# Performance work log

Measured on AMD Instinct MI355X. Metric: run time of the kernel, lower is better.

The kernel has to match this reference:

```python
import jax, jax.numpy as jnp
import numpy as np

TAU = 0.5

def setup_inputs() -> dict:
    key = jax.random.key(0)
    ks = jax.random.split(key, 6)
    B, L, D, P = 4, 4096, 256, 256
    return {
        "X1": jax.random.normal(ks[0], (B, L, D), dtype=jnp.float32),
        "X2": jax.random.normal(ks[1], (B, L, D), dtype=jnp.float32),
        "W1": jax.random.normal(ks[2], (P, D), dtype=jnp.float32) * (1.0 / np.sqrt(D)),
        "b1": jax.random.normal(ks[3], (P,), dtype=jnp.float32) * 0.01,
        "W2": jax.random.normal(ks[4], (D, P), dtype=jnp.float32) * (1.0 / np.sqrt(P)),
        "b2": jax.random.normal(ks[5], (D,), dtype=jnp.float32) * 0.01,
    }

def _projection(z, W1, b1, W2, b2):
    h = jax.nn.elu(z @ W1.T + b1)
    return h @ W2.T + b2

def _normalize(z, eps=1e-12):
    n = jnp.linalg.norm(z, axis=-1, keepdims=True)
    return z / jnp.maximum(n, eps)

def _semi_loss(z1, z2, tau):
    # z1, z2: [B, L, D]
    z1n = _normalize(z1)
    z2n = _normalize(z2)
    refl = jnp.exp(jnp.einsum('bld,bmd->blm', z1n, z1n) / tau)   # [B, L, L]
    between = jnp.exp(jnp.einsum('bld,bmd->blm', z1n, z2n) / tau)
    refl_diag = jnp.diagonal(refl, axis1=-2, axis2=-1)           # [B, L]
    between_diag = jnp.diagonal(between, axis1=-2, axis2=-1)
    denom = refl.sum(axis=-1) + between.sum(axis=-1) - refl_diag
    return -jnp.log(between_diag / denom).sum(axis=-1)           # [B]

def reference(X1, X2, W1, b1, W2, b2):
    h1 = _projection(X1, W1, b1, W2, b2)
    h2 = _projection(X2, W1, b1, W2, b2)
    l1 = _semi_loss(h1, h2, TAU)
    l2 = _semi_loss(h2, h1, TAU)
    return ((l1 + l2) * 0.5).mean()
```

## Files before the change

kernel.cpp:

```cpp
#include <hip/hip_runtime.h>
#include <math.h>


typedef __attribute__((ext_vector_type(8))) short short8;
typedef __attribute__((ext_vector_type(4))) short short4v;
typedef __attribute__((ext_vector_type(4))) float float4v;
typedef __attribute__((ext_vector_type(8))) int int8v;
typedef __attribute__((ext_vector_type(4))) int int4v;

__device__ __forceinline__ short f2bf(float f) {
    unsigned u = __builtin_bit_cast(unsigned, f);
    u += 0x7fffu + ((u >> 16) & 1u);
    return (short)(u >> 16);
}

__device__ __forceinline__ unsigned char f2fp8(float f) {
    float af = fabsf(f);
    unsigned s = (__builtin_bit_cast(unsigned, f) >> 31) << 7;
    if (af < 0.015625f) {
        int q = (int)rintf(af * 512.0f);
        return (unsigned char)(s | (unsigned)q);
    }
    unsigned au = __builtin_bit_cast(unsigned, af);
    au += 0x7FFFFu + ((au >> 20) & 1u);
    int e = (int)(au >> 23) - 127;
    unsigned m = (au >> 20) & 7u;
    return (unsigned char)(s | (unsigned)((e + 7) << 3) | m);
}

__device__ __forceinline__ void gl_lds16(const void* g, void* l) {
    __builtin_amdgcn_global_load_lds(
        (const __attribute__((address_space(1))) void*)g,
        (__attribute__((address_space(3))) void*)l, 16, 0, 0);
}

__device__ __forceinline__ void gemm256_core(
    const short* __restrict__ A, const short* __restrict__ B,
    int arow0, short* lsA, short* lsB, float4v acc[4][4])
{
    const int tid  = threadIdx.x;
    const int w    = tid >> 6;
    const int lane = tid & 63;
    const int l15  = lane & 15;

    for (int kt = 0; kt < 4; ++kt) {
        const int kbase = kt * 64;
#pragma unroll
        for (int r = 0; r < 10; ++r) {
            const int c = w * 10 + r;
            if (c < 8) {
                const int s   = c * 64 + lane;
                const int kc  = s >> 6;
                const int row = s & 63;
                gl_lds16(A + (size_t)(arow0 + row) * 256 + kbase + kc * 8,
                         lsA + (size_t)c * 512);
            } else {
                const int s   = (c - 8) * 64 + lane;
                const int kc  = s >> 8;
                const int row = s & 255;
                gl_lds16(B + (size_t)row * 256 + kbase + kc * 8,
                         lsB + (size_t)(c - 8) * 512);
            }
        }
        __syncthreads();
#pragma unroll
        for (int ks = 0; ks < 2; ++ks) {
            const int kc = ks * 4 + (lane >> 4);
            short8 af[4], bfv[4];
#pragma unroll
            for (int mi = 0; mi < 4; ++mi)
                af[mi] = *(const short8*)(lsA + ((size_t)kc * 64 + mi * 16 + l15) * 8);
#pragma unroll
            for (int ni = 0; ni < 4; ++ni)
                bfv[ni] = *(const short8*)(lsB + ((size_t)kc * 256 + w * 64 + ni * 16 + l15) * 8);
#pragma unroll
            for (int mi = 0; mi < 4; ++mi)
#pragma unroll
                for (int ni = 0; ni < 4; ++ni)
                    acc[mi][ni] = __builtin_amdgcn_mfma_f32_16x16x32_bf16(
                        af[mi], bfv[ni], acc[mi][ni], 0, 0, 0);
        }
        __syncthreads();
    }
}

__global__ __launch_bounds__(256) void convX_kernel(
    const float* __restrict__ X1, const float* __restrict__ X2,
    short* __restrict__ dst)
{
    int i = blockIdx.x * 256 + threadIdx.x;
    const float* src = (i < 1048576) ? X1 : X2;
    int j = i & 1048575;
    float4v v = ((const float4v*)src)[j];
    short4v o;
    o.x = f2bf(v.x); o.y = f2bf(v.y); o.z = f2bf(v.z); o.w = f2bf(v.w);
    ((short4v*)dst)[i] = o;
}

__global__ __launch_bounds__(256) void convW_kernel(
    const float* __restrict__ W1, const float* __restrict__ W2,
    short* __restrict__ d1, short* __restrict__ d2)
{
    int i = blockIdx.x * 256 + threadIdx.x;
    const float* src = (i < 16384) ? W1 : W2;
    short* dst = (i < 16384) ? d1 : d2;
    int j = i & 16383;
    float4v v = ((const float4v*)src)[j];
    short4v o;
    o.x = f2bf(v.x); o.y = f2bf(v.y); o.z = f2bf(v.z); o.w = f2bf(v.w);
    ((short4v*)dst)[j] = o;
}

__global__ __launch_bounds__(256, 4) void proj1_kernel(
    const short* __restrict__ Xbf, const short* __restrict__ W1bf,
    const float* __restrict__ b1, short* __restrict__ Hbf)
{
    __shared__ short lsA[4096];
    __shared__ short lsB[16384];
    const int arow0 = blockIdx.x * 64;
    float4v acc[4][4];
#pragma unroll
    for (int mi = 0; mi < 4; ++mi)
#pragma unroll
        for (int ni = 0; ni < 4; ++ni)
            acc[mi][ni] = (float4v){0.f, 0.f, 0.f, 0.f};

    gemm256_core(Xbf, W1bf, arow0, lsA, lsB, acc);

    const int tid  = threadIdx.x;
    const int w    = tid >> 6;
    const int lane = tid & 63;
    const int rowbase = arow0 + (lane >> 4) * 4;
    const int colbase = w * 64 + (lane & 15);
#pragma unroll
    for (int ni = 0; ni < 4; ++ni) {
        const int col = colbase + ni * 16;
        const float bv = b1[col];
#pragma unroll
        for (int mi = 0; mi < 4; ++mi)
#pragma unroll
            for (int reg = 0; reg < 4; ++reg) {
                const int row = rowbase + mi * 16 + reg;
                float v = acc[mi][ni][reg] + bv;
                v = (v > 0.f) ? v : expm1f(v);
                Hbf[(size_t)row * 256 + col] = f2bf(v);
            }
    }
}

__global__ __launch_bounds__(256, 4) void proj2norm_kernel(
    const short* __restrict__ Hbf, const short* __restrict__ W2bf,
    const float* __restrict__ b2, unsigned char* __restrict__ zn8)
{
    __shared__ short lsA[4096];
    __shared__ short lsB[16384];
    __shared__ float rssq[4][64];
    __shared__ float rinv[64];
    const int arow0 = blockIdx.x * 64;
    float4v acc[4][4];
#pragma unroll
    for (int mi = 0; mi < 4; ++mi)
#pragma unroll
        for (int ni = 0; ni < 4; ++ni)
            acc[mi][ni] = (float4v){0.f, 0.f, 0.f, 0.f};

    gemm256_core(Hbf, W2bf, arow0, lsA, lsB, acc);

    const int tid  = threadIdx.x;
    const int w    = tid >> 6;
    const int lane = tid & 63;
    const int quad = lane >> 4;
    const int l15  = lane & 15;

#pragma unroll
    for (int ni = 0; ni < 4; ++ni) {
        const float bv = b2[w * 64 + ni * 16 + l15];
#pragma unroll
        for (int mi = 0; mi < 4; ++mi)
#pragma unroll
            for (int reg = 0; reg < 4; ++reg)
                acc[mi][ni][reg] += bv;
    }
    float ps[4][4];
#pragma unroll
    for (int mi = 0; mi < 4; ++mi)
#pragma unroll
        for (int reg = 0; reg < 4; ++reg) {
            float s = 0.f;
#pragma unroll
            for (int ni = 0; ni < 4; ++ni) {
                float v = acc[mi][ni][reg];
                s += v * v;
            }
            s += __shfl_xor(s, 1); s += __shfl_xor(s, 2);
            s += __shfl_xor(s, 4); s += __shfl_xor(s, 8);
            ps[mi][reg] = s;
        }
    if (l15 == 0) {
#pragma unroll
        for (int mi = 0; mi < 4; ++mi)
#pragma unroll
            for (int reg = 0; reg < 4; ++reg)
                rssq[w][mi * 16 + quad * 4 + reg] = ps[mi][reg];
    }
    __syncthreads();
    if (tid < 64) {
        float ssq = rssq[0][tid] + rssq[1][tid] + rssq[2][tid] + rssq[3][tid];
        rinv[tid] = 1.41421356237f / fmaxf(sqrtf(ssq), 1e-12f);
    }
    __syncthreads();

    const int r0  = arow0;
    const int set = r0 >> 14;
    const int bb  = (r0 >> 12) & 3;
    const int l0  = r0 & 4095;
    unsigned char* dst = zn8 + ((size_t)(bb * 2 + set) * 4096 + l0) * 256;
    const int colbase = w * 64 + l15;
#pragma unroll
    for (int mi = 0; mi < 4; ++mi)
#pragma unroll
        for (int reg = 0; reg < 4; ++reg) {
            const int rl = mi * 16 + quad * 4 + reg;
            const float inv = rinv[rl];
#pragma unroll
            for (int ni = 0; ni < 4; ++ni)
                dst[(size_t)rl * 256 + colbase + ni * 16] =
                    f2fp8(acc[mi][ni][reg] * inv);
        }
}

#if defined(__has_builtin)
#if __has_builtin(__builtin_amdgcn_mfma_scale_f32_16x16x128_f8f6f4)
#define HAVE_MX 1
#endif
#endif

__global__ __launch_bounds__(256, 2) void gram_fp8_kernel(
    const unsigned char* __restrict__ zn8, float* __restrict__ S,
    float* __restrict__ out)
{
    __shared__ unsigned char lsB[2][32768];

    const int bx    = blockIdx.x;
    const int xcd   = bx & 7;
    const int batch = xcd >> 1;
    const int sub   = (bx >> 3) * 2 + (xcd & 1);
    const int stripe = sub >> 1;
    const int half   = sub & 1;
    const unsigned char* Z = zn8 + (size_t)batch * 2097152;
    const int q0 = stripe * 128;
    const int t0 = half * 32;
    const int djt = (q0 ^ 4096) >> 7;

    const int tid  = threadIdx.x;
    const int w    = tid >> 6;
    const int lane = tid & 63;
    const int wm   = w & 1;
    const int wn   = w >> 1;
    const int quad = lane >> 4;
    const int l15  = lane & 15;

#define STAGE_B(t, buf)                                                       \
    {                                                                         \
        const unsigned char* Bb = Z + (size_t)(t) * 128 * 256;                \
        _Pragma("unroll")                                                     \
        for (int r = 0; r < 8; ++r) {                                         \
            const int c   = w * 8 + r;                                        \
            const int u   = c * 64 + lane;                                    \
            const int kp  = u >> 7;                                           \
            const int col = u & 127;                                          \
            gl_lds16(Bb + (size_t)col * 256 + kp * 16,                        \
                     &lsB[buf][(size_t)c * 1024]);                            \
        }                                                                     \
    }

    float rs[4][4];
#pragma unroll
    for (int mi = 0; mi < 4; ++mi)
#pragma unroll
        for (int reg = 0; reg < 4; ++reg)
            rs[mi][reg] = 0.f;
    float dsum = 0.f;

#ifdef HAVE_MX
    int8v afr[4][2];
    {
        const unsigned char* Ab = Z + (size_t)(q0 + wm * 64) * 256;
#pragma unroll
        for (int mi = 0; mi < 4; ++mi)
#pragma unroll
            for (int ks = 0; ks < 2; ++ks) {
                const unsigned char* p = Ab + (size_t)(mi * 16 + l15) * 256
                                         + ks * 128 + quad * 32;
                int4v lo = *(const int4v*)p;
                int4v hi = *(const int4v*)(p + 16);
                afr[mi][ks] = __builtin_shufflevector(lo, hi, 0,1,2,3,4,5,6,7);
            }
    }

    STAGE_B(t0, 0);
    __syncthreads();

    for (int jt = 0; jt < 32; ++jt) {
        const int buf = jt & 1;
        if (jt < 31) STAGE_B(t0 + jt + 1, buf ^ 1);

        float4v acc[4][4];
#pragma unroll
        for (int mi = 0; mi < 4; ++mi)
#pragma unroll
            for (int ni = 0; ni < 4; ++ni)
                acc[mi][ni] = (float4v){0.f, 0.f, 0.f, 0.f};

        const unsigned char* lb = &lsB[buf][0];
#pragma unroll
        for (int ks = 0; ks < 2; ++ks) {
            const int kp0 = ks * 8 + quad * 2;
            int8v bfv[4];
#pragma unroll
            for (int ni = 0; ni < 4; ++ni) {
                const unsigned char* p = lb +
                    ((size_t)kp0 * 128 + wn * 64 + ni * 16 + l15) * 16;
                int4v lo = *(const int4v*)p;
                int4v hi = *(const int4v*)(p + 2048);
                bfv[ni] = __builtin_shufflevector(lo, hi, 0,1,2,3,4,5,6,7);
            }
#pragma unroll
            for (int mi = 0; mi < 4; ++mi)
#pragma unroll
                for (int ni = 0; ni < 4; ++ni)
                    acc[mi][ni] = __builtin_amdgcn_mfma_scale_f32_16x16x128_f8f6f4(
                        afr[mi][ks], bfv[ni], acc[mi][ni],
                        0, 0,
                        0, 0x7F7F7F7F,
                        0, 0x7F7F7F7F);
        }

        if (t0 + jt == djt) {
#pragma unroll
            for (int mi = 0; mi < 4; ++mi)
#pragma unroll
                for (int ni = 0; ni < 4; ++ni)
#pragma unroll
                    for (int reg = 0; reg < 4; ++reg) {
                        const int rg = q0 + wm * 64 + mi * 16 + quad * 4 + reg;
                        const int cg = djt * 128 + wn * 64 + ni * 16 + l15;
                        if ((rg ^ 4096) == cg) dsum += acc[mi][ni][reg];
                    }
        }

#pragma unroll
        for (int mi = 0; mi < 4; ++mi)
#pragma unroll
            for (int reg = 0; reg < 4; ++reg) {
                float s = 0.f;
#pragma unroll
                for (int ni = 0; ni < 4; ++ni)
                    s += __expf(acc[mi][ni][reg]);
                rs[mi][reg] += s;
            }

        __syncthreads();
    }
#else
    long afr[4][8];
    {
        const unsigned char* Ab = Z + (size_t)(q0 + wm * 64) * 256;
#pragma unroll
        for (int mi = 0; mi < 4; ++mi)
#pragma unroll
            for (int kc = 0; kc < 8; ++kc)
                afr[mi][kc] = *(const long*)(Ab + (size_t)(mi * 16 + l15) * 256
                                             + kc * 32 + quad * 8);
    }
    STAGE_B(t0, 0);
    __syncthreads();
    for (int jt = 0; jt < 32; ++jt) {
        const int buf = jt & 1;
        if (jt < 31) STAGE_B(t0 + jt + 1, buf ^ 1);
        float4v acc[4][4];
#pragma unroll
        for (int mi = 0; mi < 4; ++mi)
#pragma unroll
            for (int ni = 0; ni < 4; ++ni)
                acc[mi][ni] = (float4v){0.f, 0.f, 0.f, 0.f};
        const unsigned char* lb = &lsB[buf][0];
#pragma unroll
        for (int kc = 0; kc < 8; ++kc) {
            const int kseg = kc * 4 + quad;
            const int kp   = kseg >> 1;
            const int hf   = kseg & 1;
            long bfv[4];
#pragma unroll
            for (int ni = 0; ni < 4; ++ni)
                bfv[ni] = *(const long*)(lb +
                    ((size_t)kp * 128 + wn * 64 + ni * 16 + l15) * 16 + hf * 8);
#pragma unroll
            for (int mi = 0; mi < 4; ++mi)
#pragma unroll
                for (int ni = 0; ni < 4; ++ni)
                    acc[mi][ni] = __builtin_amdgcn_mfma_f32_16x16x32_fp8_fp8(
                        afr[mi][kc], bfv[ni], acc[mi][ni], 0, 0, 0);
        }
        if (t0 + jt == djt) {
#pragma unroll
            for (int mi = 0; mi < 4; ++mi)
#pragma unroll
                for (int ni = 0; ni < 4; ++ni)
#pragma unroll
                    for (int reg = 0; reg < 4; ++reg) {
                        const int rg = q0 + wm * 64 + mi * 16 + quad * 4 + reg;
                        const int cg = djt * 128 + wn * 64 + ni * 16 + l15;
                        if ((rg ^ 4096) == cg) dsum += acc[mi][ni][reg];
                    }
        }
#pragma unroll
        for (int mi = 0; mi < 4; ++mi)
#pragma unroll
            for (int reg = 0; reg < 4; ++reg) {
                float s = 0.f;
#pragma unroll
                for (int ni = 0; ni < 4; ++ni)
                    s += __expf(acc[mi][ni][reg]);
                rs[mi][reg] += s;
            }
        __syncthreads();
    }
#endif

#pragma unroll
    for (int mi = 0; mi < 4; ++mi)
#pragma unroll
        for (int reg = 0; reg < 4; ++reg) {
            float v = rs[mi][reg];
            v += __shfl_xor(v, 1); v += __shfl_xor(v, 2);
            v += __shfl_xor(v, 4); v += __shfl_xor(v, 8);
            rs[mi][reg] = v;
        }
    if (l15 == 0) {
        float* Sq = S + (size_t)batch * 8192 + q0 + wm * 64;
#pragma unroll
        for (int mi = 0; mi < 4; ++mi)
#pragma unroll
            for (int reg = 0; reg < 4; ++reg)
                atomicAdd(&Sq[mi * 16 + quad * 4 + reg], rs[mi][reg]);
    }
    {
        float dv = dsum;
        dv += __shfl_xor(dv, 1);  dv += __shfl_xor(dv, 2);
        dv += __shfl_xor(dv, 4);  dv += __shfl_xor(dv, 8);
        dv += __shfl_xor(dv, 16); dv += __shfl_xor(dv, 32);
        if (lane == 0 && dv != 0.f)
            atomicAdd(out, -0.125f * dv);
    }
#undef STAGE_B
}

__global__ __launch_bounds__(256) void final_log_kernel(
    const float* __restrict__ S, float* __restrict__ out)
{
    __shared__ float red[4];
    const int tid  = threadIdx.x;
    const int w    = tid >> 6;
    const int lane = tid & 63;
    const float E2 = 7.3890560989306495f;
    float acc = 0.f;
    for (int i = blockIdx.x * 256 + tid; i < 32768; i += gridDim.x * 256)
        acc += logf(S[i] - E2);
    acc += __shfl_xor(acc, 1);  acc += __shfl_xor(acc, 2);
    acc += __shfl_xor(acc, 4);  acc += __shfl_xor(acc, 8);
    acc += __shfl_xor(acc, 16); acc += __shfl_xor(acc, 32);
    if (lane == 0) red[w] = acc;
    __syncthreads();
    if (tid == 0)
        atomicAdd(out, 0.125f * (red[0] + red[1] + red[2] + red[3]));
}

extern "C" void kernel_launch(void* const* d_in, const int* in_sizes, int n_in,
                              void* d_out, int out_size, void* d_ws, size_t ws_size,
                              hipStream_t stream)
{
    const float* X1 = (const float*)d_in[0];
    const float* X2 = (const float*)d_in[1];
    const float* W1 = (const float*)d_in[2];
    const float* b1 = (const float*)d_in[3];
    const float* W2 = (const float*)d_in[4];
    const float* b2 = (const float*)d_in[5];

    char* ws = (char*)d_ws;
    float* S    = (float*)(ws + 0);
    short* W1bf = (short*)(ws + 131072);
    short* W2bf = (short*)(ws + 262144);
    short* Xbf  = (short*)(ws + 393216);
    unsigned char* zn8 = (unsigned char*)(ws + 393216);
    short* Hbf  = (short*)(ws + 17170432);

    hipMemsetAsync(S, 0, 131072, stream);
    hipMemsetAsync(d_out, 0, sizeof(float), stream);

    convW_kernel<<<128, 256, 0, stream>>>(W1, W2, W1bf, W2bf);
    convX_kernel<<<8192, 256, 0, stream>>>(X1, X2, Xbf);
    proj1_kernel<<<512, 256, 0, stream>>>(Xbf, W1bf, b1, Hbf);
    proj2norm_kernel<<<512, 256, 0, stream>>>(Hbf, W2bf, b2, zn8);
    gram_fp8_kernel<<<512, 256, 0, stream>>>(zn8, S, (float*)d_out);
    final_log_kernel<<<64, 256, 0, stream>>>(S, (float*)d_out);
}
```

Measured before the change: 217.3 us.

## Exploit Gram matrix symmetry with upper-triangular tiles and exp2 scaling

Replaces the row-stripe Gram kernel with one block per upper-triangular 128x128 tile of the combined 8192x8192 similarity matrix, so each off-diagonal tile's exponentials feed both its row sums and its column sums. This halves the MFMA and exp work. It also folds log2(e) into the normalisation scale so exp2 can be used directly, and rescales the diagonal term to match. The cost is many more small blocks (8320), no double-buffered staging, and roughly twice as many atomics per element. The triangular index is recovered with a sqrt plus correction loops.

New measurement: 676.2 us. +211.1%, slower.

```diff
diff --git a/kernel.cpp b/kernel.cpp
--- a/kernel.cpp
+++ b/kernel.cpp
@@ -7,6 +7,15 @@
 typedef __attribute__((ext_vector_type(4))) float float4v;
 typedef __attribute__((ext_vector_type(8))) int int8v;
 typedef __attribute__((ext_vector_type(4))) int int4v;
+
+#if defined(__has_builtin)
+#if __has_builtin(__builtin_amdgcn_exp2f)
+#define EXP2F(x) __builtin_amdgcn_exp2f(x)
+#endif
+#endif
+#ifndef EXP2F
+#define EXP2F(x) __expf(0.69314718056f * (x))
+#endif
 
 __device__ __forceinline__ short f2bf(float f) {
     unsigned u = __builtin_bit_cast(unsigned, f);
@@ -206,7 +215,7 @@
     __syncthreads();
     if (tid < 64) {
         float ssq = rssq[0][tid] + rssq[1][tid] + rssq[2][tid] + rssq[3][tid];
-        rinv[tid] = 1.41421356237f / fmaxf(sqrtf(ssq), 1e-12f);
+        rinv[tid] = 1.69864360f / fmaxf(sqrtf(ssq), 1e-12f);
     }
     __syncthreads();
 
@@ -235,22 +244,29 @@
 #endif
 #endif
 
-__global__ __launch_bounds__(256, 2) void gram_fp8_kernel(
+__global__ __launch_bounds__(256, 5) void gram_fp8_sym_kernel(
     const unsigned char* __restrict__ zn8, float* __restrict__ S,
     float* __restrict__ out)
 {
-    __shared__ unsigned char lsB[2][32768];
+    __shared__ unsigned char lsB[32768];
 
     const int bx    = blockIdx.x;
     const int xcd   = bx & 7;
     const int batch = xcd >> 1;
-    const int sub   = (bx >> 3) * 2 + (xcd & 1);
-    const int stripe = sub >> 1;
-    const int half   = sub & 1;
+    const int t     = (bx >> 3) * 2 + (xcd & 1);
+
+    int ti = (int)((129.0f - sqrtf((float)(16641 - 8 * t))) * 0.5f);
+    if (ti < 0) ti = 0;
+    if (ti > 63) ti = 63;
+    while (64 * (ti + 1) - ((ti + 1) * ti) / 2 <= t) ++ti;
+    while (64 * ti - (ti * (ti - 1)) / 2 > t) --ti;
+    const int tj = ti + (t - (64 * ti - (ti * (ti - 1)) / 2));
+
     const unsigned char* Z = zn8 + (size_t)batch * 2097152;
-    const int q0 = stripe * 128;
-    const int t0 = half * 32;
-    const int djt = (q0 ^ 4096) >> 7;
+    const int q0 = ti * 128;
+    const int c0 = tj * 128;
+    const bool offdiag = (tj > ti);
+    const bool cross   = (tj == ti + 32);
 
     const int tid  = threadIdx.x;
     const int w    = tid >> 6;
@@ -260,27 +276,24 @@
     const int quad = lane >> 4;
     const int l15  = lane & 15;
 
-#define STAGE_B(t, buf)                                                       \
-    {                                                                         \
-        const unsigned char* Bb = Z + (size_t)(t) * 128 * 256;                \
-        _Pragma("unroll")                                                     \
-        for (int r = 0; r < 8; ++r) {                                         \
-            const int c   = w * 8 + r;                                        \
-            const int u   = c * 64 + lane;                                    \
-            const int kp  = u >> 7;                                           \
-            const int col = u & 127;                                          \
-            gl_lds16(Bb + (size_t)col * 256 + kp * 16,                        \
-                     &lsB[buf][(size_t)c * 1024]);                            \
-        }                                                                     \
-    }
-
-    float rs[4][4];
-#pragma unroll
-    for (int mi = 0; mi < 4; ++mi)
-#pragma unroll
-        for (int reg = 0; reg < 4; ++reg)
-            rs[mi][reg] = 0.f;
-    float dsum = 0.f;
+    {
+        const unsigned char* Bb = Z + (size_t)c0 * 256;
+#pragma unroll
+        for (int r = 0; r < 8; ++r) {
+            const int c   = w * 8 + r;
+            const int u   = c * 64 + lane;
+            const int kp  = u >> 7;
+            const int col = u & 127;
+            gl_lds16(Bb + (size_t)col * 256 + kp * 16, &lsB[(size_t)c * 1024]);
+        }
+    }
+
+    float4v acc[4][4];
+#pragma unroll
+    for (int mi = 0; mi < 4; ++mi)
+#pragma unroll
+        for (int ni = 0; ni < 4; ++ni)
+            acc[mi][ni] = (float4v){0.f, 0.f, 0.f, 0.f};
 
 #ifdef HAVE_MX
     int8v afr[4][2];
@@ -298,21 +311,10 @@
             }
     }
 
-    STAGE_B(t0, 0);
     __syncthreads();
 
-    for (int jt = 0; jt < 32; ++jt) {
-        const int buf = jt & 1;
-        if (jt < 31) STAGE_B(t0 + jt + 1, buf ^ 1);
-
-        float4v acc[4][4];
-#pragma unroll
-        for (int mi = 0; mi < 4; ++mi)
-#pragma unroll
-            for (int ni = 0; ni < 4; ++ni)
-                acc[mi][ni] = (float4v){0.f, 0.f, 0.f, 0.f};
-
-        const unsigned char* lb = &lsB[buf][0];
+    {
+        const unsigned char* lb = &lsB[0];
 #pragma unroll
         for (int ks = 0; ks < 2; ++ks) {
             const int kp0 = ks * 8 + quad * 2;
@@ -335,32 +337,6 @@
                         0, 0x7F7F7F7F,
                         0, 0x7F7F7F7F);
         }
-
-        if (t0 + jt == djt) {
-#pragma unroll
-            for (int mi = 0; mi < 4; ++mi)
-#pragma unroll
-                for (int ni = 0; ni < 4; ++ni)
-#pragma unroll
-                    for (int reg = 0; reg < 4; ++reg) {
-                        const int rg = q0 + wm * 64 + mi * 16 + quad * 4 + reg;
-                        const int cg = djt * 128 + wn * 64 + ni * 16 + l15;
-                        if ((rg ^ 4096) == cg) dsum += acc[mi][ni][reg];
-                    }
-        }
-
-#pragma unroll
-        for (int mi = 0; mi < 4; ++mi)
-#pragma unroll
-            for (int reg = 0; reg < 4; ++reg) {
-                float s = 0.f;
-#pragma unroll
-                for (int ni = 0; ni < 4; ++ni)
-                    s += __expf(acc[mi][ni][reg]);
-                rs[mi][reg] += s;
-            }
-
-        __syncthreads();
     }
 #else
     long afr[4][8];
@@ -373,18 +349,9 @@
                 afr[mi][kc] = *(const long*)(Ab + (size_t)(mi * 16 + l15) * 256
                                              + kc * 32 + quad * 8);
     }
-    STAGE_B(t0, 0);
     __syncthreads();
-    for (int jt = 0; jt < 32; ++jt) {
-        const int buf = jt & 1;
-        if (jt < 31) STAGE_B(t0 + jt + 1, buf ^ 1);
-        float4v acc[4][4];
-#pragma unroll
-        for (int mi = 0; mi < 4; ++mi)
-#pragma unroll
-            for (int ni = 0; ni < 4; ++ni)
-                acc[mi][ni] = (float4v){0.f, 0.f, 0.f, 0.f};
-        const unsigned char* lb = &lsB[buf][0];
+    {
+        const unsigned char* lb = &lsB[0];
 #pragma unroll
         for (int kc = 0; kc < 8; ++kc) {
             const int kseg = kc * 4 + quad;
@@ -402,58 +369,70 @@
                     acc[mi][ni] = __builtin_amdgcn_mfma_f32_16x16x32_fp8_fp8(
                         afr[mi][kc], bfv[ni], acc[mi][ni], 0, 0, 0);
         }
-        if (t0 + jt == djt) {
+    }
+#endif
+
+    float dsum = 0.f;
+    if (cross) {
+#pragma unroll
+        for (int mi = 0; mi < 4; ++mi)
+#pragma unroll
+            for (int ni = 0; ni < 4; ++ni)
+#pragma unroll
+                for (int reg = 0; reg < 4; ++reg) {
+                    const int r = wm * 64 + mi * 16 + quad * 4 + reg;
+                    const int c = wn * 64 + ni * 16 + l15;
+                    if (r == c) dsum += acc[mi][ni][reg];
+                }
+    }
+
+#pragma unroll
+    for (int mi = 0; mi < 4; ++mi)
+#pragma unroll
+        for (int ni = 0; ni < 4; ++ni)
+#pragma unroll
+            for (int reg = 0; reg < 4; ++reg)
+                acc[mi][ni][reg] = EXP2F(acc[mi][ni][reg]);
+
+    {
+        float* Sr = S + (size_t)batch * 8192 + q0 + wm * 64;
+#pragma unroll
+        for (int mi = 0; mi < 4; ++mi)
+#pragma unroll
+            for (int reg = 0; reg < 4; ++reg) {
+                float s = acc[mi][0][reg] + acc[mi][1][reg]
+                        + acc[mi][2][reg] + acc[mi][3][reg];
+                s += __shfl_xor(s, 1); s += __shfl_xor(s, 2);
+                s += __shfl_xor(s, 4); s += __shfl_xor(s, 8);
+                if (l15 == 0)
+                    atomicAdd(&Sr[mi * 16 + quad * 4 + reg], s);
+            }
+    }
+
+    if (offdiag) {
+        float* Sc = S + (size_t)batch * 8192 + c0 + wn * 64;
+#pragma unroll
+        for (int ni = 0; ni < 4; ++ni) {
+            float s = 0.f;
 #pragma unroll
             for (int mi = 0; mi < 4; ++mi)
 #pragma unroll
-                for (int ni = 0; ni < 4; ++ni)
-#pragma unroll
-                    for (int reg = 0; reg < 4; ++reg) {
-                        const int rg = q0 + wm * 64 + mi * 16 + quad * 4 + reg;
-                        const int cg = djt * 128 + wn * 64 + ni * 16 + l15;
-                        if ((rg ^ 4096) == cg) dsum += acc[mi][ni][reg];
-                    }
-        }
-#pragma unroll
-        for (int mi = 0; mi < 4; ++mi)
-#pragma unroll
-            for (int reg = 0; reg < 4; ++reg) {
-                float s = 0.f;
-#pragma unroll
-                for (int ni = 0; ni < 4; ++ni)
-                    s += __expf(acc[mi][ni][reg]);
-                rs[mi][reg] += s;
-            }
-        __syncthreads();
-    }
-#endif
-
-#pragma unroll
-    for (int mi = 0; mi < 4; ++mi)
-#pragma unroll
-        for (int reg = 0; reg < 4; ++reg) {
-            float v = rs[mi][reg];
-            v += __shfl_xor(v, 1); v += __shfl_xor(v, 2);
-            v += __shfl_xor(v, 4); v += __shfl_xor(v, 8);
-            rs[mi][reg] = v;
-        }
-    if (l15 == 0) {
-        float* Sq = S + (size_t)batch * 8192 + q0 + wm * 64;
-#pragma unroll
-        for (int mi = 0; mi < 4; ++mi)
-#pragma unroll
-            for (int reg = 0; reg < 4; ++reg)
-                atomicAdd(&Sq[mi * 16 + quad * 4 + reg], rs[mi][reg]);
-    }
-    {
+                for (int reg = 0; reg < 4; ++reg)
+                    s += acc[mi][ni][reg];
+            s += __shfl_xor(s, 16); s += __shfl_xor(s, 32);
+            if (quad == 0)
+                atomicAdd(&Sc[ni * 16 + l15], s);
+        }
+    }
+
+    if (cross) {
         float dv = dsum;
         dv += __shfl_xor(dv, 1);  dv += __shfl_xor(dv, 2);
         dv += __shfl_xor(dv, 4);  dv += __shfl_xor(dv, 8);
         dv += __shfl_xor(dv, 16); dv += __shfl_xor(dv, 32);
-        if (lane == 0 && dv != 0.f)
-            atomicAdd(out, -0.125f * dv);
-    }
-#undef STAGE_B
+        if (lane == 0)
+            atomicAdd(out, -0.17328680f * dv);
+    }
 }
 
 __global__ __launch_bounds__(256) void final_log_kernel(
@@ -502,6 +481,6 @@
     convX_kernel<<<8192, 256, 0, stream>>>(X1, X2, Xbf);
     proj1_kernel<<<512, 256, 0, stream>>>(Xbf, W1bf, b1, Hbf);
     proj2norm_kernel<<<512, 256, 0, stream>>>(Hbf, W2bf, b2, zn8);
-    gram_fp8_kernel<<<512, 256, 0, stream>>>(zn8, S, (float*)d_out);
+    gram_fp8_sym_kernel<<<8320, 256, 0, stream>>>(zn8, S, (float*)d_out);
     final_log_kernel<<<64, 256, 0, stream>>>(S, (float*)d_out);
 }
```
